# Optimization experiments

Measured on AMD Instinct MI355X. Metric: run time of the kernel, lower is better.

The kernel has to match this reference:

```python
import jax, jax.numpy as jnp
import numpy as np
import itertools

N_PARTICLES = 8388608
GRID_RES = 2048
BOX_SIZE = 1000.0

def _rotations_47():
    perms = list(itertools.permutations([0, 1, 2]))
    signs = list(itertools.product([1, -1], repeat=3))
    mats = []
    for s in signs:
        for p in perms:
            M = np.zeros((3, 3), np.float32)
            M[0, p[0]] = s[0]; M[1, p[1]] = s[1]; M[2, p[2]] = s[2]
            mats.append(M)
    return jnp.asarray(np.stack(mats)[1:])  # drop identity -> 47 matrices

# Analytic stand-ins for jax_cosmo background quantities (EdS-like forms).
def _Gp(a):
    return a ** 1.5

def _dGfa(a):
    return 1.5 * jnp.sqrt(a)

def _a_of_chi(chi):
    return 1.0 / (1.0 + chi / 3000.0)

def _paint_2d(pos, center, width, box_size, res):
    """CIC scatter of particles inside a z-slab onto a [res,res] density plane."""
    z = pos[:, 2]
    sel = ((z >= center - width * 0.5) & (z < center + width * 0.5)).astype(pos.dtype)
    xy = pos[:, :2] * (res / box_size)          # grid coordinates, [N,2]
    i0 = jnp.floor(xy)
    f = xy - i0                                  # CIC fractional offsets
    i0 = i0.astype(jnp.int32)
    ix0 = jnp.mod(i0[:, 0], res); iy0 = jnp.mod(i0[:, 1], res)
    ix1 = jnp.mod(i0[:, 0] + 1, res); iy1 = jnp.mod(i0[:, 1] + 1, res)
    fx, fy = f[:, 0], f[:, 1]
    flat = jnp.zeros((res * res,), dtype=pos.dtype)
    flat = flat.at[ix0 * res + iy0].add(sel * (1 - fx) * (1 - fy))
    flat = flat.at[ix1 * res + iy0].add(sel * fx * (1 - fy))
    flat = flat.at[ix0 * res + iy1].add(sel * (1 - fx) * fy)
    flat = flat.at[ix1 * res + iy1].add(sel * fx * fy)
    return flat.reshape(res, res)

def setup_inputs():
    key = jax.random.key(0)
    k1, k2 = jax.random.split(key)
    positions = jax.random.uniform(k1, (N_PARTICLES, 3), jnp.float32) * BOX_SIZE
    velocities = jax.random.normal(k2, (N_PARTICLES, 3), jnp.float32) * 2.0
    return {
        "positions": positions,
        "velocities": velocities,
        "rotations": _rotations_47(),
        "observer": jnp.zeros((3,), jnp.float32),
        "r_centers": jnp.asarray([250.0, 750.0, 1250.0, 1750.0], jnp.float32),
        "density_widths": jnp.full((4,), 500.0, jnp.float32),
        "t": jnp.float32(0.8),
        "max_comoving_distance": jnp.float32(BOX_SIZE),
        "box_size": jnp.float32(BOX_SIZE),
        "shell_idx": 2,
        "rotation_idx": 1,
        "grid_res": GRID_RES,
    }

def reference(positions, velocities, rotations, observer, r_centers, density_widths,
              t, max_comoving_distance, box_size, shell_idx, rotation_idx, grid_res):
    r_center = r_centers[shell_idx]
    width = density_widths[shell_idx]
    inside_box = r_center + width * 0.5 <= max_comoving_distance

    def inside_branch(args):
        pos, _vel = args
        return _paint_2d(pos, r_center, width, box_size, grid_res)

    def telephoto_branch(args):
        pos, vel = args
        M = rotations[rotation_idx % 47]                                   # [3,3]
        shift = jnp.floor(r_center / max_comoving_distance) * max_comoving_distance
        p_rot = (pos - observer) @ M.T                                      # rotate about observer
        z_axis = jnp.array([0.0, 0.0, 1.0], pos.dtype)
        p_shift = p_rot + z_axis * shift
        v_rot = vel @ M.T
        dist = jnp.linalg.norm(p_shift - observer, axis=-1)                 # [N]
        a_tgt = _a_of_chi(dist)[:, None]                                    # per-particle target scale factor
        ac = jnp.sqrt(t * a_tgt)
        drift = (_Gp(a_tgt) - _Gp(t)) / _dGfa(ac)
        p_drift = p_shift + drift * v_rot
        return _paint_2d(p_drift + observer, r_center, width, box_size, grid_res)

    return jax.lax.cond(inside_box, inside_branch, telephoto_branch, (positions, velocities))
```

## Files before the change

kernel.cpp:

```cpp
#include <hip/hip_runtime.h>
#include <cmath>


#define TSZ    128
#define NBKT   256
#define NXCC   8
#define CAP    4096
#define DEPTH  22
#define NTH    256
#define NBLK   1536
#define VEC    4
#define NSUB   2
#define DESCMAX 256

__device__ __forceinline__ int get_xcc_id() {
    int x = __builtin_amdgcn_s_getreg((3 << 11) | (0 << 6) | 20);
    return x & (NXCC - 1);
}

__device__ __forceinline__ float fast_rcp(float x)  { return __builtin_amdgcn_rcpf(x); }
__device__ __forceinline__ float fast_sqrt(float x) { return __builtin_amdgcn_sqrtf(x); }

__device__ __forceinline__ int wrap_idx(int v, int res) {
    v += (v < 0) ? res : 0;
    v += (v < 0) ? res : 0;
    v += (v < 0) ? res : 0;
    v -= (v >= res) ? res : 0;
    v -= (v >= res) ? res : 0;
    v -= (v >= res) ? res : 0;
    if (v < 0 || v >= res) { v %= res; if (v < 0) v += res; }
    return v;
}

__device__ __forceinline__ void scatter_direct(float* __restrict__ out, int res,
                                               int gx0, int gy0, float fx, float fy) {
    int gx1 = gx0 + 1; if (gx1 >= res) gx1 = 0;
    int gy1 = gy0 + 1; if (gy1 >= res) gy1 = 0;
    atomicAdd(&out[gx0 * res + gy0], (1.0f - fx) * (1.0f - fy));
    atomicAdd(&out[gx1 * res + gy0], fx * (1.0f - fy));
    atomicAdd(&out[gx0 * res + gy1], (1.0f - fx) * fy);
    atomicAdd(&out[gx1 * res + gy1], fx * fy);
}

__device__ __forceinline__ void rec_decode(unsigned rec, int b, int tiles,
                                           int& gx, int& gy, float& fx, float& fy) {
    int tx = b / tiles, ty = b - tx * tiles;
    gx = (tx << 7) + (int)(rec >> 25);
    gy = (ty << 7) + (int)((rec >> 18) & 127u);
    fx = (float)((rec >> 9) & 511u) * (1.0f / 512.0f);
    fy = (float)(rec & 511u) * (1.0f / 512.0f);
}

struct Uni {
    float m00, m01, m02, m10, m11, m12, m20, m21, m22;
    float ox, oy, oz, shift;
    float r_lo, r_hi, t, gp_t, scale;
    int   resm1, res, tiles;
    bool  inside;
};

struct PR {
    unsigned rec, st;
    int ix0, iy0;
    float fx, fy;
    bool val;
};

__device__ __forceinline__ PR tp_compute(
    const Uni& u, unsigned dummy,
    float px, float py, float pz, float vx, float vy, float vz)
{
    float X, Y, Z;
    if (u.inside) {
        X = px; Y = py; Z = pz;
    } else {
        const float qx_ = px - u.ox, qy_ = py - u.oy, qz_ = pz - u.oz;
        float rx = u.m00 * qx_ + u.m01 * qy_ + u.m02 * qz_;
        float ry = u.m10 * qx_ + u.m11 * qy_ + u.m12 * qz_;
        float rz = u.m20 * qx_ + u.m21 * qy_ + u.m22 * qz_ + u.shift;

        const float vrx = u.m00 * vx + u.m01 * vy + u.m02 * vz;
        const float vry = u.m10 * vx + u.m11 * vy + u.m12 * vz;
        const float vrz = u.m20 * vx + u.m21 * vy + u.m22 * vz;

        const float dx = rx - u.ox, dy = ry - u.oy, dz = rz - u.oz;
        const float dist  = fast_sqrt(dx * dx + dy * dy + dz * dz);
        const float a_tgt = fast_rcp(1.0f + dist * (1.0f / 3000.0f));
        const float ac    = fast_sqrt(u.t * a_tgt);
        const float gp_a  = a_tgt * fast_sqrt(a_tgt);
        const float drift = (gp_a - u.gp_t) * fast_rcp(1.5f * fast_sqrt(ac));

        X = rx + drift * vrx + u.ox;
        Y = ry + drift * vry + u.oy;
        Z = rz + drift * vrz + u.oz;
    }
    PR o;
    o.val = (Z >= u.r_lo && Z < u.r_hi);

    const float gx = X * u.scale, gy = Y * u.scale;
    const float fgx = floorf(gx), fgy = floorf(gy);
    o.fx = gx - fgx; o.fy = gy - fgy;
    o.ix0 = ((int)fgx) & u.resm1;
    o.iy0 = ((int)fgy) & u.resm1;
    const unsigned st = (unsigned)((o.ix0 >> 7) * u.tiles + (o.iy0 >> 7));
    o.st = o.val ? st : dummy;

    unsigned qx = (unsigned)(o.fx * 512.0f + 0.5f); if (qx > 511u) qx = 511u;
    unsigned qy = (unsigned)(o.fy * 512.0f + 0.5f); if (qy > 511u) qy = 511u;
    o.rec = ((unsigned)(o.ix0 & 127) << 25) | ((unsigned)(o.iy0 & 127) << 18)
          | (qx << 9) | qy;
    return o;
}

__device__ __forceinline__ void tp_finish(
    const Uni& u, const PR& o, unsigned p,
    unsigned* __restrict__ fill, unsigned* __restrict__ buf,
    float* __restrict__ out)
{
    if (!o.val) return;
    if (p < DEPTH) buf[o.st * DEPTH + p] = o.rec;
    else { atomicSub(&fill[o.st], 1u); scatter_direct(out, u.res, o.ix0, o.iy0, o.fx, o.fy); }
}

__device__ __forceinline__ void tp_process(
    const Uni& u, float px, float py, float pz, float vx, float vy, float vz,
    unsigned* __restrict__ fill, unsigned* __restrict__ buf,
    float* __restrict__ out)
{
    const PR o = tp_compute(u, 0u, px, py, pz, vx, vy, vz);
    if (!o.val) return;
    unsigned p = atomicAdd(&fill[o.st], 1u);
    tp_finish(u, o, p, fill, buf, out);
}

__global__ __launch_bounds__(NTH, 6) void tp_bin(
    const float* __restrict__ pos, const float* __restrict__ vel,
    const float* __restrict__ rotations, const float* __restrict__ observer,
    const float* __restrict__ r_centers, const float* __restrict__ widths,
    const float* __restrict__ t_p, const float* __restrict__ maxd_p,
    const float* __restrict__ box_p, const int* __restrict__ shell_p,
    const int* __restrict__ ridx_p,
    unsigned* __restrict__ gcnt, unsigned* __restrict__ grec,
    float* __restrict__ out, int res, int tiles, int n, int rounds)
{
    __shared__ unsigned fill[NBKT + 64];
    __shared__ unsigned buf[NBKT * DEPTH];
    __shared__ unsigned descB[DESCMAX];
    __shared__ unsigned descD[DESCMAX];
    __shared__ unsigned ndesc;

    const int tid = threadIdx.x;
    for (int b = tid; b < NBKT + 64; b += NTH) fill[b] = 0;
    if (tid == 0) ndesc = 0;

    Uni u;
    {
        const int   shell    = shell_p[0];
        const float r_center = r_centers[shell];
        const float width    = widths[shell];
        const float maxd     = maxd_p[0];
        const float box      = box_p[0];
        u.t      = t_p[0];
        u.inside = (r_center + width * 0.5f) <= maxd;
        int ridx = ridx_p[0] % 47; if (ridx < 0) ridx += 47;
        const float* M = rotations + 9 * ridx;
        u.m00 = M[0]; u.m01 = M[1]; u.m02 = M[2];
        u.m10 = M[3]; u.m11 = M[4]; u.m12 = M[5];
        u.m20 = M[6]; u.m21 = M[7]; u.m22 = M[8];
        u.ox = observer[0]; u.oy = observer[1]; u.oz = observer[2];
        u.shift = floorf(r_center / maxd) * maxd;
        u.r_lo = r_center - width * 0.5f;
        u.r_hi = r_center + width * 0.5f;
        u.gp_t = u.t * sqrtf(u.t);
        u.scale = (float)res / box;
        u.resm1 = res - 1; u.res = res; u.tiles = tiles;
    }

    const int xcc = get_xcc_id();
    const int segbase = xcc * NBKT;
    const unsigned dummy = (unsigned)(NBKT + (tid & 63));
    const float4* __restrict__ pos4 = (const float4*)pos;
    const float4* __restrict__ vel4 = (const float4*)vel;

    __syncthreads();

    for (int r = 0; r < rounds; ++r) {
        #pragma unroll 1
        for (int s = 0; s < NSUB; ++s) {
            const int rc = r * NSUB + s;
            const int base = ((rc * NBLK + blockIdx.x) * NTH + tid) * VEC;
            if (base + VEC <= n) {
                const int q = base * 3 / 4;
                const float4 a = pos4[q], b = pos4[q + 1], c = pos4[q + 2];
                PR r0, r1, r2, r3;
                if (u.inside) {
                    r0 = tp_compute(u, dummy, a.x, a.y, a.z, 0, 0, 0);
                    r1 = tp_compute(u, dummy, a.w, b.x, b.y, 0, 0, 0);
                    r2 = tp_compute(u, dummy, b.z, b.w, c.x, 0, 0, 0);
                    r3 = tp_compute(u, dummy, c.y, c.z, c.w, 0, 0, 0);
                } else {
                    const float4 d = vel4[q], e = vel4[q + 1], f = vel4[q + 2];
                    r0 = tp_compute(u, dummy, a.x, a.y, a.z, d.x, d.y, d.z);
                    r1 = tp_compute(u, dummy, a.w, b.x, b.y, d.w, e.x, e.y);
                    r2 = tp_compute(u, dummy, b.z, b.w, c.x, e.z, e.w, f.x);
                    r3 = tp_compute(u, dummy, c.y, c.z, c.w, f.y, f.z, f.w);
                }
                const unsigned p0 = atomicAdd(&fill[r0.st], 1u);
                const unsigned p1 = atomicAdd(&fill[r1.st], 1u);
                const unsigned p2 = atomicAdd(&fill[r2.st], 1u);
                const unsigned p3 = atomicAdd(&fill[r3.st], 1u);
                tp_finish(u, r0, p0, fill, buf, out);
                tp_finish(u, r1, p1, fill, buf, out);
                tp_finish(u, r2, p2, fill, buf, out);
                tp_finish(u, r3, p3, fill, buf, out);
            } else {
                for (int p = 0; p < VEC; ++p) {
                    const int i = base + p;
                    if (i >= 0 && i < n)
                        tp_process(u, pos[3 * i], pos[3 * i + 1], pos[3 * i + 2],
                                   vel[3 * i], vel[3 * i + 1], vel[3 * i + 2],
                                   fill, buf, out);
                }
            }
        }
        __syncthreads();
        if (tid < NBKT) {
            const unsigned c = fill[tid];
            const unsigned k = c >> 4;
            if (k) {
                unsigned gbase = atomicAdd(&gcnt[segbase + tid], 16u * k);
                unsigned d = atomicAdd(&ndesc, k);
                for (unsigned g = 0; g < k; ++g) {
                    descB[d + g] = (unsigned)tid | ((g * 16u) << 16);
                    descD[d + g] = gbase + 16u * g;
                }
            }
        }
        __syncthreads();
        const unsigned nd = ndesc;
        for (unsigned did = (unsigned)(tid >> 4); did < nd; did += NTH / 16) {
            const unsigned e = descB[did];
            const unsigned b = e & 0xffffu, so = e >> 16;
            const unsigned dst = descD[did] + (unsigned)(tid & 15);
            const unsigned rv = buf[b * DEPTH + so + (tid & 15)];
            if (dst < CAP) {
                grec[(size_t)(segbase + b) * CAP + dst] = rv;
            } else {
                int gx0, gy0; float ffx, ffy;
                rec_decode(rv, (int)b, u.tiles, gx0, gy0, ffx, ffy);
                scatter_direct(out, u.res, gx0, gy0, ffx, ffy);
            }
        }
        __syncthreads();
        if (tid < NBKT) {
            const unsigned c = fill[tid];
            const unsigned k = c >> 4;
            if (k) {
                const unsigned resid = c - 16u * k;
                for (unsigned j = 0; j < resid; ++j)
                    buf[tid * DEPTH + j] = buf[tid * DEPTH + 16u * k + j];
                fill[tid] = resid;
            }
        }
        if (tid == 0) ndesc = 0;
        __syncthreads();
    }

    if (tid < NBKT) {
        const unsigned c = fill[tid];
        if (c) {
            unsigned d = atomicAdd(&ndesc, 1u);
            unsigned gbase = atomicAdd(&gcnt[segbase + tid], c);
            descB[d] = (unsigned)tid | (c << 16);
            descD[d] = gbase;
        }
    }
    __syncthreads();
    const unsigned nd = ndesc;
    for (unsigned did = (unsigned)(tid >> 4); did < nd; did += NTH / 16) {
        const unsigned e = descB[did];
        const unsigned b = e & 0xffffu, c = e >> 16;
        const unsigned lane = (unsigned)(tid & 15);
        if (lane < c) {
            const unsigned dst = descD[did] + lane;
            const unsigned rv = buf[b * DEPTH + lane];
            if (dst < CAP) {
                grec[(size_t)(segbase + b) * CAP + dst] = rv;
            } else {
                int gx0, gy0; float ffx, ffy;
                rec_decode(rv, (int)b, u.tiles, gx0, gy0, ffx, ffy);
                scatter_direct(out, u.res, gx0, gy0, ffx, ffy);
            }
        }
    }
}

__global__ __launch_bounds__(1024) void tp_paint(
    const unsigned* __restrict__ gcnt, const unsigned* __restrict__ grec,
    float* __restrict__ out, int res, int tiles)
{
    __shared__ unsigned long long quad[4][64 * 64];
    const int b = blockIdx.x;
    const int tx = b / tiles, ty = b - tx * tiles;

    for (int c = threadIdx.x; c < 4 * 64 * 64; c += blockDim.x)
        quad[c >> 12][c & 4095] = 0ull;
    __syncthreads();

    for (int x = 0; x < NXCC; ++x) {
        unsigned m = gcnt[x * NBKT + b]; if (m > CAP) m = CAP;
        const unsigned* rr = grec + (size_t)(x * NBKT + b) * CAP;
        for (unsigned k = threadIdx.x; k < m; k += blockDim.x) {
            const unsigned p = rr[k];
            const int li = (int)(p >> 25);
            const int lj = (int)((p >> 18) & 127u);
            const unsigned qx = (p >> 9) & 511u;
            const unsigned qy = p & 511u;
            const unsigned ax = 512u - qx, ay = 512u - qy;
            const unsigned long long w00 = (ax * ay + 128u) >> 8;
            const unsigned long long w01 = (ax * qy + 128u) >> 8;
            const unsigned long long w10 = (qx * ay + 128u) >> 8;
            const unsigned long long w11 = (qx * qy + 128u) >> 8;
            const unsigned long long pk = w00 | (w01 << 16) | (w10 << 32) | (w11 << 48);
            const int g = ((li & 1) << 1) | (lj & 1);
            atomicAdd(&quad[g][(li >> 1) * 64 + (lj >> 1)], pk);
        }
    }
    __syncthreads();

    for (int c = threadIdx.x; c < (TSZ + 1) * (TSZ + 1); c += blockDim.x) {
        const int i = c / (TSZ + 1), j = c - i * (TSZ + 1);
        unsigned acc = 0;
        #pragma unroll
        for (int r = 0; r < 2; ++r) {
            const int ii = i - r;
            if (ii < 0 || ii > TSZ - 1) continue;
            #pragma unroll
            for (int s = 0; s < 2; ++s) {
                const int jj = j - s;
                if (jj < 0 || jj > TSZ - 1) continue;
                const int g = ((ii & 1) << 1) | (jj & 1);
                const unsigned long long v = quad[g][(ii >> 1) * 64 + (jj >> 1)];
                acc += (unsigned)((v >> (16 * (r * 2 + s))) & 0xffffull);
            }
        }
        const float val = (float)acc * (1.0f / 1024.0f);
        int gx = tx * TSZ + i; if (gx >= res) gx -= res;
        int gy = ty * TSZ + j; if (gy >= res) gy -= res;
        float* dst = &out[gx * res + gy];
        if (i == 0 || j == 0 || i == TSZ || j == TSZ) {
            if (val != 0.0f) atomicAdd(dst, val);
        } else {
            *dst += val;
        }
    }
}

__global__ __launch_bounds__(256) void tp_direct(
    const float* __restrict__ pos, const float* __restrict__ vel,
    const float* __restrict__ rotations, const float* __restrict__ observer,
    const float* __restrict__ r_centers, const float* __restrict__ widths,
    const float* __restrict__ t_p, const float* __restrict__ maxd_p,
    const float* __restrict__ box_p, const int* __restrict__ shell_p,
    const int* __restrict__ ridx_p, float* __restrict__ out, int res, int n)
{
    int i = blockIdx.x * blockDim.x + threadIdx.x;
    if (i >= n) return;
    const int   shell    = shell_p[0];
    const float r_center = r_centers[shell];
    const float width    = widths[shell];
    const float maxd     = maxd_p[0];
    const float box      = box_p[0];
    const float t        = t_p[0];
    const bool  inside   = (r_center + width * 0.5f) <= maxd;
    int ridx = ridx_p[0] % 47; if (ridx < 0) ridx += 47;

    float px = pos[3 * i], py = pos[3 * i + 1], pz = pos[3 * i + 2];
    float X, Y, Z;
    if (inside) {
        X = px; Y = py; Z = pz;
    } else {
        const float* M = rotations + 9 * ridx;
        const float ox = observer[0], oy = observer[1], oz = observer[2];
        const float qx = px - ox, qy = py - oy, qz = pz - oz;
        float rx = M[0] * qx + M[1] * qy + M[2] * qz;
        float ry = M[3] * qx + M[4] * qy + M[5] * qz;
        float rz = M[6] * qx + M[7] * qy + M[8] * qz + floorf(r_center / maxd) * maxd;
        const float vx = vel[3 * i], vy = vel[3 * i + 1], vz = vel[3 * i + 2];
        const float vrx = M[0] * vx + M[1] * vy + M[2] * vz;
        const float vry = M[3] * vx + M[4] * vy + M[5] * vz;
        const float vrz = M[6] * vx + M[7] * vy + M[8] * vz;
        const float dx = rx - ox, dy = ry - oy, dz = rz - oz;
        const float dist  = sqrtf(dx * dx + dy * dy + dz * dz);
        const float a_tgt = 1.0f / (1.0f + dist / 3000.0f);
        const float ac    = sqrtf(t * a_tgt);
        const float drift = (a_tgt * sqrtf(a_tgt) - t * sqrtf(t)) / (1.5f * sqrtf(ac));
        X = rx + drift * vrx + ox;
        Y = ry + drift * vry + oy;
        Z = rz + drift * vrz + oz;
    }
    if (!(Z >= r_center - width * 0.5f && Z < r_center + width * 0.5f)) return;

    const float scale = (float)res / box;
    const float gx = X * scale, gy = Y * scale;
    const float fgx = floorf(gx), fgy = floorf(gy);
    scatter_direct(out, res, wrap_idx((int)fgx, res), wrap_idx((int)fgy, res),
                   gx - fgx, gy - fgy);
}

extern "C" void kernel_launch(void* const* d_in, const int* in_sizes, int n_in,
                              void* d_out, int out_size, void* d_ws, size_t ws_size,
                              hipStream_t stream) {
    const float* pos   = (const float*)d_in[0];
    const float* velv  = (const float*)d_in[1];
    const float* rot   = (const float*)d_in[2];
    const float* obs   = (const float*)d_in[3];
    const float* rc    = (const float*)d_in[4];
    const float* dw    = (const float*)d_in[5];
    const float* t     = (const float*)d_in[6];
    const float* maxd  = (const float*)d_in[7];
    const float* box   = (const float*)d_in[8];
    const int*   shell = (const int*)d_in[9];
    const int*   ridx  = (const int*)d_in[10];
    float* out = (float*)d_out;

    const int n   = in_sizes[0] / 3;
    const int res = (int)llround(sqrt((double)out_size));

    hipMemsetAsync(out, 0, (size_t)out_size * sizeof(float), stream);

    const int tiles = res / TSZ;
    const int nt2 = tiles * tiles;
    const size_t cnt_bytes = (size_t)NXCC * NBKT * sizeof(unsigned);
    const size_t rec_bytes = (size_t)NXCC * NBKT * CAP * sizeof(unsigned);
    const bool pow2 = res > 0 && (res & (res - 1)) == 0;

    if (!pow2 || res % TSZ != 0 || nt2 > NBKT ||
        (long long)res * res != (long long)out_size ||
        ws_size < cnt_bytes + rec_bytes) {
        tp_direct<<<(n + 255) / 256, 256, 0, stream>>>(
            pos, velv, rot, obs, rc, dw, t, maxd, box, shell, ridx, out, res, n);
        return;
    }

    unsigned* gcnt = (unsigned*)d_ws;
    unsigned* grec = (unsigned*)((char*)d_ws + cnt_bytes);

    hipMemsetAsync(gcnt, 0, cnt_bytes, stream);

    const int per_round = NBLK * NTH * VEC * NSUB;
    const int rounds = (n + per_round - 1) / per_round;
    tp_bin<<<NBLK, NTH, 0, stream>>>(
        pos, velv, rot, obs, rc, dw, t, maxd, box, shell, ridx,
        gcnt, grec, out, res, tiles, n, rounds);

    tp_paint<<<nt2, 1024, 0, stream>>>(gcnt, grec, out, res, tiles);
}
```

Baseline: 284.5 us.

## Replace global atomic bin counters with fixed per-block record slots and byte counts

Removes the per-XCC global atomic counters and the counter memset. Each bin kernel block now writes its records into private fixed slots (two 16-record chunks per bucket) plus a per-block byte count, and overflow falls back to direct atomic scatter. The paint kernel loads all per-block counts into LDS, then scans every slot and masks out the unused ones. Block count, sub-rounds, LDS depth and launch bounds are retuned to match. This trades global atomic contention for scanning mostly-empty slots and risks more direct-scatter overflow when blocks exceed two chunks per bucket.

```diff
diff --git a/kernel.cpp b/kernel.cpp
--- a/kernel.cpp
+++ b/kernel.cpp
@@ -4,19 +4,15 @@
 
 #define TSZ    128
 #define NBKT   256
-#define NXCC   8
-#define CAP    4096
-#define DEPTH  22
+#define CAPB   2
+#define SLOTS  (CAPB*16)
+#define DEPTH  26
 #define NTH    256
-#define NBLK   1536
+#define NBLK   960
 #define VEC    4
-#define NSUB   2
+#define NSUB   3
 #define DESCMAX 256
-
-__device__ __forceinline__ int get_xcc_id() {
-    int x = __builtin_amdgcn_s_getreg((3 << 11) | (0 << 6) | 20);
-    return x & (NXCC - 1);
-}
+#define SENT   0xFFFFFFFFu
 
 __device__ __forceinline__ float fast_rcp(float x)  { return __builtin_amdgcn_rcpf(x); }
 __device__ __forceinline__ float fast_sqrt(float x) { return __builtin_amdgcn_sqrtf(x); }
@@ -133,24 +129,26 @@
     tp_finish(u, o, p, fill, buf, out);
 }
 
-__global__ __launch_bounds__(NTH, 6) void tp_bin(
+__global__ __launch_bounds__(NTH) void tp_bin(
     const float* __restrict__ pos, const float* __restrict__ vel,
     const float* __restrict__ rotations, const float* __restrict__ observer,
     const float* __restrict__ r_centers, const float* __restrict__ widths,
     const float* __restrict__ t_p, const float* __restrict__ maxd_p,
     const float* __restrict__ box_p, const int* __restrict__ shell_p,
     const int* __restrict__ ridx_p,
-    unsigned* __restrict__ gcnt, unsigned* __restrict__ grec,
+    unsigned char* __restrict__ cnts, unsigned* __restrict__ grec,
     float* __restrict__ out, int res, int tiles, int n, int rounds)
 {
     __shared__ unsigned fill[NBKT + 64];
     __shared__ unsigned buf[NBKT * DEPTH];
     __shared__ unsigned descB[DESCMAX];
     __shared__ unsigned descD[DESCMAX];
+    __shared__ unsigned char cidA[NBKT];
     __shared__ unsigned ndesc;
 
     const int tid = threadIdx.x;
     for (int b = tid; b < NBKT + 64; b += NTH) fill[b] = 0;
+    if (tid < NBKT) cidA[tid] = 0;
     if (tid == 0) ndesc = 0;
 
     Uni u;
@@ -176,8 +174,6 @@
         u.resm1 = res - 1; u.res = res; u.tiles = tiles;
     }
 
-    const int xcc = get_xcc_id();
-    const int segbase = xcc * NBKT;
     const unsigned dummy = (unsigned)(NBKT + (tid & 63));
     const float4* __restrict__ pos4 = (const float4*)pos;
     const float4* __restrict__ vel4 = (const float4*)vel;
@@ -228,12 +224,16 @@
             const unsigned c = fill[tid];
             const unsigned k = c >> 4;
             if (k) {
-                unsigned gbase = atomicAdd(&gcnt[segbase + tid], 16u * k);
                 unsigned d = atomicAdd(&ndesc, k);
+                unsigned cid = cidA[tid];
                 for (unsigned g = 0; g < k; ++g) {
                     descB[d + g] = (unsigned)tid | ((g * 16u) << 16);
-                    descD[d + g] = gbase + 16u * g;
+                    descD[d + g] = (cid < CAPB)
+                        ? (unsigned)(((unsigned)tid * NBLK + blockIdx.x) * SLOTS + cid * 16u)
+                        : SENT;
+                    ++cid;
                 }
+                cidA[tid] = (unsigned char)cid;
             }
         }
         __syncthreads();
@@ -241,10 +241,10 @@
         for (unsigned did = (unsigned)(tid >> 4); did < nd; did += NTH / 16) {
             const unsigned e = descB[did];
             const unsigned b = e & 0xffffu, so = e >> 16;
-            const unsigned dst = descD[did] + (unsigned)(tid & 15);
             const unsigned rv = buf[b * DEPTH + so + (tid & 15)];
-            if (dst < CAP) {
-                grec[(size_t)(segbase + b) * CAP + dst] = rv;
+            const unsigned dstb = descD[did];
+            if (dstb != SENT) {
+                grec[(size_t)dstb + (tid & 15)] = rv;
             } else {
                 int gx0, gy0; float ffx, ffy;
                 rec_decode(rv, (int)b, u.tiles, gx0, gy0, ffx, ffy);
@@ -268,11 +268,16 @@
 
     if (tid < NBKT) {
         const unsigned c = fill[tid];
+        const unsigned cid = cidA[tid];
+        const unsigned wc = (cid < CAPB) ? cid : (unsigned)CAPB;
+        const bool rw = (c > 0) && (cid < CAPB);
+        cnts[(size_t)blockIdx.x * NBKT + tid] = (unsigned char)(16u * wc + (rw ? c : 0u));
         if (c) {
             unsigned d = atomicAdd(&ndesc, 1u);
-            unsigned gbase = atomicAdd(&gcnt[segbase + tid], c);
             descB[d] = (unsigned)tid | (c << 16);
-            descD[d] = gbase;
+            descD[d] = rw
+                ? (unsigned)(((unsigned)tid * NBLK + blockIdx.x) * SLOTS + cid * 16u)
+                : SENT;
         }
     }
     __syncthreads();
@@ -282,10 +287,10 @@
         const unsigned b = e & 0xffffu, c = e >> 16;
         const unsigned lane = (unsigned)(tid & 15);
         if (lane < c) {
-            const unsigned dst = descD[did] + lane;
             const unsigned rv = buf[b * DEPTH + lane];
-            if (dst < CAP) {
-                grec[(size_t)(segbase + b) * CAP + dst] = rv;
+            const unsigned dstb = descD[did];
+            if (dstb != SENT) {
+                grec[(size_t)dstb + lane] = rv;
             } else {
                 int gx0, gy0; float ffx, ffy;
                 rec_decode(rv, (int)b, u.tiles, gx0, gy0, ffx, ffy);
@@ -296,22 +301,25 @@
 }
 
 __global__ __launch_bounds__(1024) void tp_paint(
-    const unsigned* __restrict__ gcnt, const unsigned* __restrict__ grec,
+    const unsigned char* __restrict__ cnts, const unsigned* __restrict__ grec,
     float* __restrict__ out, int res, int tiles)
 {
     __shared__ unsigned long long quad[4][64 * 64];
+    __shared__ unsigned char cs[NBLK];
     const int b = blockIdx.x;
     const int tx = b / tiles, ty = b - tx * tiles;
 
     for (int c = threadIdx.x; c < 4 * 64 * 64; c += blockDim.x)
         quad[c >> 12][c & 4095] = 0ull;
+    for (int i = threadIdx.x; i < NBLK; i += blockDim.x)
+        cs[i] = cnts[(size_t)i * NBKT + b];
     __syncthreads();
 
-    for (int x = 0; x < NXCC; ++x) {
-        unsigned m = gcnt[x * NBKT + b]; if (m > CAP) m = CAP;
-        const unsigned* rr = grec + (size_t)(x * NBKT + b) * CAP;
-        for (unsigned k = threadIdx.x; k < m; k += blockDim.x) {
-            const unsigned p = rr[k];
+    const unsigned* __restrict__ rr = grec + (size_t)b * NBLK * SLOTS;
+    const int total = NBLK * SLOTS;
+    for (int idx = threadIdx.x; idx < total; idx += blockDim.x) {
+        const unsigned p = rr[idx];
+        if ((idx & (SLOTS - 1)) < (int)cs[idx >> 5]) {
             const int li = (int)(p >> 25);
             const int lj = (int)((p >> 18) & 127u);
             const unsigned qx = (p >> 9) & 511u;
@@ -431,28 +439,26 @@
 
     const int tiles = res / TSZ;
     const int nt2 = tiles * tiles;
-    const size_t cnt_bytes = (size_t)NXCC * NBKT * sizeof(unsigned);
-    const size_t rec_bytes = (size_t)NXCC * NBKT * CAP * sizeof(unsigned);
+    const size_t rec_bytes = (size_t)NBKT * NBLK * SLOTS * sizeof(unsigned);
+    const size_t cnt_bytes = (size_t)NBLK * NBKT;
     const bool pow2 = res > 0 && (res & (res - 1)) == 0;
 
     if (!pow2 || res % TSZ != 0 || nt2 > NBKT ||
         (long long)res * res != (long long)out_size ||
-        ws_size < cnt_bytes + rec_bytes) {
+        ws_size < rec_bytes + cnt_bytes) {
         tp_direct<<<(n + 255) / 256, 256, 0, stream>>>(
             pos, velv, rot, obs, rc, dw, t, maxd, box, shell, ridx, out, res, n);
         return;
     }
 
-    unsigned* gcnt = (unsigned*)d_ws;
-    unsigned* grec = (unsigned*)((char*)d_ws + cnt_bytes);
-
-    hipMemsetAsync(gcnt, 0, cnt_bytes, stream);
+    unsigned* grec = (unsigned*)d_ws;
+    unsigned char* cnts = (unsigned char*)d_ws + rec_bytes;
 
     const int per_round = NBLK * NTH * VEC * NSUB;
     const int rounds = (n + per_round - 1) / per_round;
     tp_bin<<<NBLK, NTH, 0, stream>>>(
         pos, velv, rot, obs, rc, dw, t, maxd, box, shell, ridx,
-        gcnt, grec, out, res, tiles, n, rounds);
-
-    tp_paint<<<nt2, 1024, 0, stream>>>(gcnt, grec, out, res, tiles);
-}
+        cnts, grec, out, res, tiles, n, rounds);
+
+    tp_paint<<<nt2, 1024, 0, stream>>>(cnts, grec, out, res, tiles);
+}
```

New measurement: 295.3 us. +3.8%, slower.
